# Kernel tuning notes

Measured on AMD Instinct MI355X. Metric: run time of the kernel, lower is better.

The kernel has to match this reference:

```python
import jax, jax.numpy as jnp
import numpy as np

FEATS = 1024
HEAD = 16
MLP_HIDDEN = 4096
HEAD_DIM = FEATS // HEAD
SQRT_D = float(FEATS) ** 0.5  # module scales by sqrt(feats), not sqrt(head_dim)
LN_EPS = 1e-5


def layer_norm(x, g, b):
    mu = jnp.mean(x, axis=-1, keepdims=True)
    var = jnp.mean(jnp.square(x - mu), axis=-1, keepdims=True)
    return (x - mu) * jax.lax.rsqrt(var + LN_EPS) * g + b


def setup_inputs() -> dict:
    key = jax.random.key(0)
    ks = jax.random.split(key, 12)
    s = 1.0 / np.sqrt(FEATS)
    s2 = 1.0 / np.sqrt(MLP_HIDDEN)
    return {
        "x": jax.random.normal(ks[0], (2, 2048, FEATS), dtype=jnp.float32),
        "ln1_g": jnp.ones((FEATS,), jnp.float32),
        "ln1_b": jnp.zeros((FEATS,), jnp.float32),
        "wq": jax.random.normal(ks[1], (FEATS, FEATS), jnp.float32) * s,
        "bq": jnp.zeros((FEATS,), jnp.float32),
        "wk": jax.random.normal(ks[2], (FEATS, FEATS), jnp.float32) * s,
        "bk": jnp.zeros((FEATS,), jnp.float32),
        "wv": jax.random.normal(ks[3], (FEATS, FEATS), jnp.float32) * s,
        "bv": jnp.zeros((FEATS,), jnp.float32),
        "wo": jax.random.normal(ks[4], (FEATS, FEATS), jnp.float32) * s,
        "bo": jnp.zeros((FEATS,), jnp.float32),
        "ln2_g": jnp.ones((FEATS,), jnp.float32),
        "ln2_b": jnp.zeros((FEATS,), jnp.float32),
        "w1": jax.random.normal(ks[5], (MLP_HIDDEN, FEATS), jnp.float32) * s,
        "b1": jnp.zeros((MLP_HIDDEN,), jnp.float32),
        "w2": jax.random.normal(ks[6], (FEATS, MLP_HIDDEN), jnp.float32) * s2,
        "b2": jnp.zeros((FEATS,), jnp.float32),
    }


def reference(x, ln1_g, ln1_b, wq, bq, wk, bk, wv, bv, wo, bo,
              ln2_g, ln2_b, w1, b1, w2, b2):
    b, n, f = x.shape
    h = layer_norm(x, ln1_g, ln1_b)
    # qkv projections (torch Linear: y = x @ W.T + b)
    q = (h @ wq.T + bq).reshape(b, n, HEAD, HEAD_DIM).transpose(0, 2, 1, 3)
    k = (h @ wk.T + bk).reshape(b, n, HEAD, HEAD_DIM).transpose(0, 2, 1, 3)
    v = (h @ wv.T + bv).reshape(b, n, HEAD, HEAD_DIM).transpose(0, 2, 1, 3)
    score = jax.nn.softmax(jnp.einsum('bhif,bhjf->bhij', q, k) / SQRT_D, axis=-1)
    attn = jnp.einsum('bhij,bhjf->bihf', score, v).reshape(b, n, f)
    o = attn @ wo.T + bo
    out1 = o + x
    h2 = layer_norm(out1, ln2_g, ln2_b)
    mlp = jax.nn.relu(jax.nn.relu(h2 @ w1.T + b1) @ w2.T + b2)
    return mlp + out1
```

## Files before the change

### kernel.cpp

```cpp
#include <hip/hip_runtime.h>
#include <hip/hip_bf16.h>

#define FEATS 1024
#define NH 16
#define HD 64
#define SEQ 2048
#define BATCH 2
#define MTOT (BATCH*SEQ)
#define MLPH 4096
#define QSCALE 0.04508422277369218f

typedef __attribute__((ext_vector_type(8))) short bf16x8;
typedef __attribute__((ext_vector_type(4))) short bf16x4;
typedef __attribute__((ext_vector_type(4))) float f32x4;

static_assert(sizeof(bf16x8) == 16, "bf16x8 must be 16B");

__device__ __forceinline__ unsigned short f2bf(float f) {
    unsigned int u = __float_as_uint(f);
    unsigned int lsb = (u >> 16) & 1u;
    u += 0x7fffu + lsb;
    return (unsigned short)(u >> 16);
}

#define ASYNC16(GP, LP) __builtin_amdgcn_global_load_lds( \
    (const __attribute__((address_space(1))) void*)(GP),  \
    (__attribute__((address_space(3))) void*)(LP), 16, 0, 0)

__global__ __launch_bounds__(256) void cvt_all_kernel(
    const float* __restrict__ wq, const float* __restrict__ wk,
    const float* __restrict__ wv, const float* __restrict__ wo,
    const float* __restrict__ w1, const float* __restrict__ w2,
    unsigned short* __restrict__ dst) {
    const size_t i = ((size_t)blockIdx.x * 256 + threadIdx.x) * 4;
    const size_t MB = (size_t)1024 * 1024;
    const float* s;
    size_t off;
    float sc = 1.0f;
    if (i < MB)            { s = wq; off = i;          sc = QSCALE; }
    else if (i < 2 * MB)   { s = wk; off = i - MB; }
    else if (i < 3 * MB)   { s = wv; off = i - 2 * MB; }
    else if (i < 4 * MB)   { s = wo; off = i - 3 * MB; }
    else if (i < 8 * MB)   { s = w1; off = i - 4 * MB; }
    else                   { s = w2; off = i - 8 * MB; }
    float4 v = *(const float4*)(s + off);
    ushort4 o;
    o.x = f2bf(v.x * sc); o.y = f2bf(v.y * sc);
    o.z = f2bf(v.z * sc); o.w = f2bf(v.w * sc);
    *(ushort4*)(dst + i) = o;
}

__global__ __launch_bounds__(256) void concat3_kernel(const float* __restrict__ a,
                                                      const float* __restrict__ b,
                                                      const float* __restrict__ c,
                                                      float* __restrict__ o) {
    int i = blockIdx.x * 256 + threadIdx.x;
    float v = (i < 1024) ? a[i] * QSCALE : ((i < 2048) ? b[i - 1024] : c[i - 2048]);
    o[i] = v;
}

__global__ __launch_bounds__(256) void ln_kernel(const float* __restrict__ x,
                                                 const float* __restrict__ g,
                                                 const float* __restrict__ bta,
                                                 unsigned short* __restrict__ h) {
    __shared__ float red[8];
    const int row = blockIdx.x;
    const int t = threadIdx.x;
    const float* xr = x + (size_t)row * FEATS;
    float4 v = ((const float4*)xr)[t];
    float s  = v.x + v.y + v.z + v.w;
    float ss = v.x * v.x + v.y * v.y + v.z * v.z + v.w * v.w;
#pragma unroll
    for (int off = 1; off < 64; off <<= 1) {
        s  += __shfl_xor(s, off);
        ss += __shfl_xor(ss, off);
    }
    const int w = t >> 6;
    if ((t & 63) == 0) { red[w] = s; red[4 + w] = ss; }
    __syncthreads();
    s  = red[0] + red[1] + red[2] + red[3];
    ss = red[4] + red[5] + red[6] + red[7];
    const float mu  = s * (1.f / FEATS);
    const float var = ss * (1.f / FEATS) - mu * mu;
    const float rs  = rsqrtf(var + 1e-5f);
    float4 gv = ((const float4*)g)[t];
    float4 bv = ((const float4*)bta)[t];
    ushort4 ov;
    ov.x = f2bf((v.x - mu) * rs * gv.x + bv.x);
    ov.y = f2bf((v.y - mu) * rs * gv.y + bv.y);
    ov.z = f2bf((v.z - mu) * rs * gv.z + bv.z);
    ov.w = f2bf((v.w - mu) * rs * gv.w + bv.w);
    ((ushort4*)h)[(size_t)row * (FEATS / 4) + t] = ov;
}

template <bool RELU, bool ADD, bool OUTBF16>
__global__ __launch_bounds__(256, 3)
void gemm_kernel(const unsigned short* __restrict__ A,
                 const unsigned short* __restrict__ W,
                 const float* __restrict__ bias,
                 const float* __restrict__ addend,
                 void* __restrict__ outp,
                 int M, int N, int K, int gx) {
    __shared__ unsigned short lds[3][2][128 * 32];

    const int t = threadIdx.x;
    const int w = t >> 6, lane = t & 63;
    const int wr = w >> 1, wc = w & 1;
    const int li = lane & 15, lj = lane >> 4;

    const int nwg = gridDim.x;
    const int cpx = nwg >> 3;
    const int wg = blockIdx.x;
    const int swz = (wg & 7) * cpx + (wg >> 3);
    const int mb = (swz / gx) * 128, nb = (swz % gx) * 128;

    const int srow = lane >> 2;
    const int scg = ((lane & 3) ^ (srow & 3)) * 8;
    const unsigned short* gA = A + (size_t)(mb + w * 16 + srow) * K + scg;
    const unsigned short* gB = W + (size_t)(nb + w * 16 + srow) * K + scg;
    const size_t half = (size_t)64 * K;
    const int lbase = w * 512 + lane * 8;

    const int rsw = (lj ^ (li & 3)) * 8;

    const int nt = K >> 5;

#define STAGE(BUF, K0)                                             \
    do {                                                           \
        unsigned short* la_ = &lds[BUF][0][lbase];                 \
        unsigned short* lb_ = &lds[BUF][1][lbase];                 \
        ASYNC16(gA + (K0), la_);                                   \
        ASYNC16(gA + half + (K0), la_ + 2048);                     \
        ASYNC16(gB + (K0), lb_);                                   \
        ASYNC16(gB + half + (K0), lb_ + 2048);                     \
    } while (0)

    STAGE(0, 0);
    STAGE(1, 32);
    asm volatile("s_waitcnt vmcnt(4)" ::: "memory");
    __builtin_amdgcn_s_barrier();

    f32x4 acc[4][4] = {};

    for (int i = 0; i < nt; ++i) {
        const int cur = i % 3;
        const unsigned short* Al = &lds[cur][0][0];
        const unsigned short* Bl = &lds[cur][1][0];

        bf16x8 af[4], bfr[4];
#pragma unroll
        for (int m = 0; m < 4; m++)
            af[m] = *(const bf16x8*)(Al + (wr * 64 + m * 16 + li) * 32 + rsw);
#pragma unroll
        for (int n = 0; n < 4; n++)
            bfr[n] = *(const bf16x8*)(Bl + (wc * 64 + n * 16 + li) * 32 + rsw);

        const int pf = i + 2 < nt;
        if (pf) STAGE((i + 2) % 3, (i + 2) * 32);

#pragma unroll
        for (int m = 0; m < 4; m++)
#pragma unroll
            for (int n = 0; n < 4; n++)
                acc[m][n] = __builtin_amdgcn_mfma_f32_16x16x32_bf16(af[m], bfr[n], acc[m][n], 0, 0, 0);

        if (i + 1 < nt) {
            if (pf) asm volatile("s_waitcnt vmcnt(4)" ::: "memory");
            else    asm volatile("s_waitcnt vmcnt(0)" ::: "memory");
            __builtin_amdgcn_s_barrier();
        }
    }
#undef STAGE

#pragma unroll
    for (int m = 0; m < 4; m++) {
#pragma unroll
        for (int n = 0; n < 4; n++) {
            const int col = nb + wc * 64 + n * 16 + li;
            const float bv = bias[col];
#pragma unroll
            for (int r = 0; r < 4; r++) {
                const int row = mb + wr * 64 + m * 16 + lj * 4 + r;
                float v = acc[m][n][r] + bv;
                if (RELU) v = fmaxf(v, 0.f);
                if (ADD)  v += addend[(size_t)row * N + col];
                if (OUTBF16)
                    ((unsigned short*)outp)[(size_t)row * N + col] = f2bf(v);
                else
                    ((float*)outp)[(size_t)row * N + col] = v;
            }
        }
    }
}

__global__ __launch_bounds__(256) void vtrans_kernel(const unsigned short* __restrict__ qkv,
                                                     unsigned short* __restrict__ vt) {
    constexpr int LDV = 68;
    __shared__ unsigned short Vl[64 * LDV];
    const int bh = blockIdx.x, st = blockIdx.y;
    const int b = bh >> 4, h = bh & 15;
    const int t = threadIdx.x;
    const unsigned short* src = qkv + (size_t)(b * SEQ + st * 64) * (3 * FEATS) + 2 * FEATS + h * HD;
#pragma unroll
    for (int i = 0; i < 2; i++) {
        int idx = t + i * 256;
        int r = idx >> 3, c = (idx & 7) * 8;
        *(bf16x8*)(Vl + r * LDV + c) = *(const bf16x8*)(src + (size_t)r * (3 * FEATS) + c);
    }
    __syncthreads();
    unsigned short* dst = vt + (size_t)bh * HD * SEQ + st * 64;
#pragma unroll
    for (int i = 0; i < 2; i++) {
        int idx = t + i * 256;
        int d = idx >> 3, s8 = (idx & 7) * 8;
        bf16x8 v;
#pragma unroll
        for (int j = 0; j < 8; j++) v[j] = Vl[(s8 + j) * LDV + d];
        *(bf16x8*)(dst + (size_t)d * SEQ + s8) = v;
    }
}

__global__ __launch_bounds__(512, 4)
void attn_kernel(const unsigned short* __restrict__ qkv,
                 const unsigned short* __restrict__ vt,
                 unsigned short* __restrict__ out) {
    constexpr int LK = 72;
    constexpr int LV = 136;
    __shared__ unsigned short Kl[2][128 * LK];
    __shared__ unsigned short Vtl[2][64 * LV];

    const int bh = blockIdx.x;
    const int b = bh >> 4, h = bh & 15;
    const int q0 = blockIdx.y * 128;
    const int t = threadIdx.x, w = t >> 6, lane = t & 63;
    const int li = lane & 15, lj = lane >> 4;

    const size_t rstr = 3 * FEATS;
    const unsigned short* qkvb = qkv + (size_t)(b * SEQ) * rstr;
    const unsigned short* ksrc = qkvb + FEATS + h * HD;
    const unsigned short* vsrc = vt + (size_t)bh * HD * SEQ;

    bf16x8 aq[2];
#pragma unroll
    for (int kk = 0; kk < 2; kk++)
        aq[kk] = *(const bf16x8*)(qkvb + (size_t)(q0 + w * 16 + li) * rstr + h * HD + kk * 32 + lj * 8);

    f32x4 o[4] = {};
    float lsum = 0.f;

    const int skey = t >> 2, sc = (t & 3) * 16;
    const unsigned short* kg = ksrc + (size_t)skey * rstr + sc;
    const int ldoK = skey * LK + sc;
    const int sd = t >> 3, c0 = (t & 7) * 16;
    const unsigned short* vg = vsrc + (size_t)sd * SEQ + c0;
    const int posA = (c0 & 96) | (((c0 >> 2) & 3) << 3) | (((c0 >> 4) & 1) << 2);
    const int ldoV = sd * LV + posA;

    const int nt = SEQ / 128;

#define VSPLIT(VR0, VR1, BUF)                                            \
    do {                                                                 \
        *(bf16x4*)(&Vtl[BUF][ldoV])      = __builtin_shufflevector(VR0, VR0, 0, 1, 2, 3); \
        *(bf16x4*)(&Vtl[BUF][ldoV + 8])  = __builtin_shufflevector(VR0, VR0, 4, 5, 6, 7); \
        *(bf16x4*)(&Vtl[BUF][ldoV + 16]) = __builtin_shufflevector(VR1, VR1, 0, 1, 2, 3); \
        *(bf16x4*)(&Vtl[BUF][ldoV + 24]) = __builtin_shufflevector(VR1, VR1, 4, 5, 6, 7); \
    } while (0)

    {
        bf16x8 k0 = *(const bf16x8*)kg;
        bf16x8 k1 = *(const bf16x8*)(kg + 8);
        bf16x8 v0 = *(const bf16x8*)vg;
        bf16x8 v1 = *(const bf16x8*)(vg + 8);
        *(bf16x8*)(&Kl[0][ldoK])     = k0;
        *(bf16x8*)(&Kl[0][ldoK + 8]) = k1;
        VSPLIT(v0, v1, 0);
    }

    int cur = 0;
    for (int i = 0; i < nt; ++i) {
        bf16x8 kr0, kr1, vr0, vr1;
        if (i + 1 < nt) {
            const unsigned short* kn = kg + (size_t)(i + 1) * 128 * rstr;
            const unsigned short* vn = vg + (i + 1) * 128;
            kr0 = *(const bf16x8*)kn;
            kr1 = *(const bf16x8*)(kn + 8);
            vr0 = *(const bf16x8*)vn;
            vr1 = *(const bf16x8*)(vn + 8);
        }

        asm volatile("s_waitcnt lgkmcnt(0)" ::: "memory");
        __builtin_amdgcn_s_barrier();

        const unsigned short* Kc = Kl[cur];
        const unsigned short* Vc = Vtl[cur];

        f32x4 s[8];
        __builtin_amdgcn_s_setprio(1);
#pragma unroll
        for (int n = 0; n < 8; n++) {
            bf16x8 k0 = *(const bf16x8*)(Kc + (n * 16 + li) * LK + lj * 8);
            bf16x8 k1 = *(const bf16x8*)(Kc + (n * 16 + li) * LK + 32 + lj * 8);
            f32x4 acc = {};
            acc = __builtin_amdgcn_mfma_f32_16x16x32_bf16(k0, aq[0], acc, 0, 0, 0);
            acc = __builtin_amdgcn_mfma_f32_16x16x32_bf16(k1, aq[1], acc, 0, 0, 0);
            s[n] = acc;
        }
        __builtin_amdgcn_s_setprio(0);

        bf16x8 A[4];
#pragma unroll
        for (int kk = 0; kk < 4; kk++) {
            float p[8];
#pragma unroll
            for (int r = 0; r < 4; r++) {
                p[r]     = exp2f(s[2 * kk][r]);
                p[4 + r] = exp2f(s[2 * kk + 1][r]);
                lsum += p[r] + p[4 + r];
            }
            union { unsigned u[4]; bf16x8 v; } Au;
            asm("v_cvt_pk_bf16_f32 %0, %1, %2" : "=v"(Au.u[0]) : "v"(p[0]), "v"(p[1]));
            asm("v_cvt_pk_bf16_f32 %0, %1, %2" : "=v"(Au.u[1]) : "v"(p[2]), "v"(p[3]));
            asm("v_cvt_pk_bf16_f32 %0, %1, %2" : "=v"(Au.u[2]) : "v"(p[4]), "v"(p[5]));
            asm("v_cvt_pk_bf16_f32 %0, %1, %2" : "=v"(Au.u[3]) : "v"(p[6]), "v"(p[7]));
            A[kk] = Au.v;
        }

        __builtin_amdgcn_s_setprio(1);
#pragma unroll
        for (int n = 0; n < 4; n++) {
#pragma unroll
            for (int kk = 0; kk < 4; kk++) {
                bf16x8 bv = *(const bf16x8*)(Vc + (n * 16 + li) * LV + kk * 32 + lj * 8);
                o[n] = __builtin_amdgcn_mfma_f32_16x16x32_bf16(A[kk], bv, o[n], 0, 0, 0);
            }
        }
        __builtin_amdgcn_s_setprio(0);

        if (i + 1 < nt) {
            *(bf16x8*)(&Kl[cur ^ 1][ldoK])     = kr0;
            *(bf16x8*)(&Kl[cur ^ 1][ldoK + 8]) = kr1;
            VSPLIT(vr0, vr1, cur ^ 1);
        }
        cur ^= 1;
    }
#undef VSPLIT

    lsum += __shfl_xor(lsum, 16);
    lsum += __shfl_xor(lsum, 32);
    const float dinv = 1.f / lsum;
    float inv[4];
#pragma unroll
    for (int r = 0; r < 4; r++)
        inv[r] = __shfl(dinv, lj * 4 + r);

    unsigned short* ob = out + (size_t)(b * SEQ + q0 + w * 16) * FEATS + h * HD;
#pragma unroll
    for (int n = 0; n < 4; n++)
#pragma unroll
        for (int r = 0; r < 4; r++)
            ob[(size_t)(lj * 4 + r) * FEATS + n * 16 + li] = f2bf(o[n][r] * inv[r]);
}

extern "C" void kernel_launch(void* const* d_in, const int* in_sizes, int n_in,
                              void* d_out, int out_size, void* d_ws, size_t ws_size,
                              hipStream_t stream) {
    const float* x     = (const float*)d_in[0];
    const float* ln1_g = (const float*)d_in[1];
    const float* ln1_b = (const float*)d_in[2];
    const float* wq    = (const float*)d_in[3];
    const float* bq    = (const float*)d_in[4];
    const float* wk    = (const float*)d_in[5];
    const float* bk    = (const float*)d_in[6];
    const float* wv    = (const float*)d_in[7];
    const float* bvv   = (const float*)d_in[8];
    const float* wo    = (const float*)d_in[9];
    const float* bo    = (const float*)d_in[10];
    const float* ln2_g = (const float*)d_in[11];
    const float* ln2_b = (const float*)d_in[12];
    const float* w1    = (const float*)d_in[13];
    const float* b1    = (const float*)d_in[14];
    const float* w2    = (const float*)d_in[15];
    const float* b2    = (const float*)d_in[16];

    unsigned short* wqkv_b = (unsigned short*)d_ws;
    unsigned short* wo_b   = wqkv_b + 3072 * 1024;
    unsigned short* w1_b   = wo_b + 1024 * 1024;
    unsigned short* w2_b   = w1_b + 4096 * 1024;
    float*          bqkv   = (float*)(w2_b + 1024 * 4096);
    unsigned short* region = (unsigned short*)(bqkv + 3072);
    unsigned short* qkvb   = region;
    unsigned short* hb     = region + (size_t)4096 * 3072;
    unsigned short* vtb    = hb;
    unsigned short* a1     = region;
    unsigned short* attn_o = region + (size_t)4096 * 4096;
    unsigned short* h2     = attn_o;
    float*          out1   = (float*)(attn_o + (size_t)4096 * 1024);
    float*          outf   = (float*)d_out;

    dim3 blk(256);

    cvt_all_kernel<<<12288, blk, 0, stream>>>(wq, wk, wv, wo, w1, w2, wqkv_b);
    concat3_kernel<<<12, blk, 0, stream>>>(bq, bk, bvv, bqkv);

    ln_kernel<<<MTOT, blk, 0, stream>>>(x, ln1_g, ln1_b, hb);

    gemm_kernel<false, false, true><<<768, blk, 0, stream>>>(
        hb, wqkv_b, bqkv, nullptr, qkvb, MTOT, 3072, FEATS, 24);

    vtrans_kernel<<<dim3(BATCH * NH, SEQ / 64), blk, 0, stream>>>(qkvb, vtb);

    attn_kernel<<<dim3(BATCH * NH, SEQ / 128), dim3(512), 0, stream>>>(qkvb, vtb, attn_o);

    gemm_kernel<false, true, false><<<256, blk, 0, stream>>>(
        attn_o, wo_b, bo, x, out1, MTOT, FEATS, FEATS, 8);

    ln_kernel<<<MTOT, blk, 0, stream>>>(out1, ln2_g, ln2_b, h2);

    gemm_kernel<true, false, true><<<1024, blk, 0, stream>>>(
        h2, w1_b, b1, nullptr, a1, MTOT, MLPH, FEATS, 32);

    gemm_kernel<true, true, false><<<256, blk, 0, stream>>>(
        a1, w2_b, b2, out1, outf, MTOT, FEATS, MLPH, 8);
}
```

Measured before the change: 236.0 us.

## Halve attention block to 4 waves each handling 32 query rows

The attention kernel now launches 256 threads instead of 512, and each wave processes two 16-row query tiles. Each K and V fragment read from LDS is therefore reused across two MFMA streams, and each thread loads twice as much K/V per tile. The row-sum of probabilities is now computed with an extra MFMA against a vector of ones instead of scalar adds and cross-lane shuffles, and it is summed over the bf16-rounded probabilities. The cost is higher register pressure per wave and fewer waves per block available to hide latency.

```diff
diff --git a/kernel.cpp b/kernel.cpp
--- a/kernel.cpp
+++ b/kernel.cpp
@@ -220,7 +220,7 @@
     }
 }
 
-__global__ __launch_bounds__(512, 4)
+__global__ __launch_bounds__(256, 2)
 void attn_kernel(const unsigned short* __restrict__ qkv,
                  const unsigned short* __restrict__ vt,
                  unsigned short* __restrict__ out) {
@@ -240,52 +240,76 @@
     const unsigned short* ksrc = qkvb + FEATS + h * HD;
     const unsigned short* vsrc = vt + (size_t)bh * HD * SEQ;
 
-    bf16x8 aq[2];
-#pragma unroll
-    for (int kk = 0; kk < 2; kk++)
-        aq[kk] = *(const bf16x8*)(qkvb + (size_t)(q0 + w * 16 + li) * rstr + h * HD + kk * 32 + lj * 8);
-
-    f32x4 o[4] = {};
-    float lsum = 0.f;
-
-    const int skey = t >> 2, sc = (t & 3) * 16;
-    const unsigned short* kg = ksrc + (size_t)skey * rstr + sc;
-    const int ldoK = skey * LK + sc;
-    const int sd = t >> 3, c0 = (t & 7) * 16;
-    const unsigned short* vg = vsrc + (size_t)sd * SEQ + c0;
-    const int posA = (c0 & 96) | (((c0 >> 2) & 3) << 3) | (((c0 >> 4) & 1) << 2);
-    const int ldoV = sd * LV + posA;
+    bf16x8 aq[2][2];
+#pragma unroll
+    for (int hh = 0; hh < 2; hh++)
+#pragma unroll
+        for (int kk = 0; kk < 2; kk++)
+            aq[hh][kk] = *(const bf16x8*)(qkvb +
+                (size_t)(q0 + w * 32 + hh * 16 + li) * rstr + h * HD + kk * 32 + lj * 8);
+
+    f32x4 o[2][4] = {};
+    f32x4 oS[2] = {};
+
+    const short onebf = (short)0x3F80;
+    const bf16x8 ones = {onebf, onebf, onebf, onebf, onebf, onebf, onebf, onebf};
+
+    const int skey = t >> 1, dbase = (t & 1) * 32;
+    const unsigned short* kg = ksrc + (size_t)skey * rstr + dbase;
+    const int ldoK = skey * LK + dbase;
+    const int sd = t >> 2, kbase = (t & 3) * 32;
+    const unsigned short* vg = vsrc + (size_t)sd * SEQ + kbase;
+    const int ldoV = sd * LV + kbase;
 
     const int nt = SEQ / 128;
 
-#define VSPLIT(VR0, VR1, BUF)                                            \
-    do {                                                                 \
-        *(bf16x4*)(&Vtl[BUF][ldoV])      = __builtin_shufflevector(VR0, VR0, 0, 1, 2, 3); \
-        *(bf16x4*)(&Vtl[BUF][ldoV + 8])  = __builtin_shufflevector(VR0, VR0, 4, 5, 6, 7); \
-        *(bf16x4*)(&Vtl[BUF][ldoV + 16]) = __builtin_shufflevector(VR1, VR1, 0, 1, 2, 3); \
-        *(bf16x4*)(&Vtl[BUF][ldoV + 24]) = __builtin_shufflevector(VR1, VR1, 4, 5, 6, 7); \
+#define KW(BUF, R0, R1, R2, R3)                          \
+    do {                                                 \
+        *(bf16x8*)(&Kl[BUF][ldoK])      = R0;            \
+        *(bf16x8*)(&Kl[BUF][ldoK + 8])  = R1;            \
+        *(bf16x8*)(&Kl[BUF][ldoK + 16]) = R2;            \
+        *(bf16x8*)(&Kl[BUF][ldoK + 24]) = R3;            \
+    } while (0)
+#define VW1(BUF, VR, POS)                                                              \
+    do {                                                                               \
+        *(bf16x4*)(&Vtl[BUF][(POS)])     = __builtin_shufflevector(VR, VR, 0, 1, 2, 3);\
+        *(bf16x4*)(&Vtl[BUF][(POS) + 8]) = __builtin_shufflevector(VR, VR, 4, 5, 6, 7);\
+    } while (0)
+#define VW(BUF, V0, V1, V2, V3)                          \
+    do {                                                 \
+        VW1(BUF, V0, ldoV);                              \
+        VW1(BUF, V1, ldoV + 16);                         \
+        VW1(BUF, V2, ldoV + 4);                          \
+        VW1(BUF, V3, ldoV + 20);                         \
     } while (0)
 
     {
         bf16x8 k0 = *(const bf16x8*)kg;
         bf16x8 k1 = *(const bf16x8*)(kg + 8);
+        bf16x8 k2 = *(const bf16x8*)(kg + 16);
+        bf16x8 k3 = *(const bf16x8*)(kg + 24);
         bf16x8 v0 = *(const bf16x8*)vg;
         bf16x8 v1 = *(const bf16x8*)(vg + 8);
-        *(bf16x8*)(&Kl[0][ldoK])     = k0;
-        *(bf16x8*)(&Kl[0][ldoK + 8]) = k1;
-        VSPLIT(v0, v1, 0);
+        bf16x8 v2 = *(const bf16x8*)(vg + 16);
+        bf16x8 v3 = *(const bf16x8*)(vg + 24);
+        KW(0, k0, k1, k2, k3);
+        VW(0, v0, v1, v2, v3);
     }
 
     int cur = 0;
     for (int i = 0; i < nt; ++i) {
-        bf16x8 kr0, kr1, vr0, vr1;
+        bf16x8 kr0, kr1, kr2, kr3, vr0, vr1, vr2, vr3;
         if (i + 1 < nt) {
             const unsigned short* kn = kg + (size_t)(i + 1) * 128 * rstr;
             const unsigned short* vn = vg + (i + 1) * 128;
             kr0 = *(const bf16x8*)kn;
             kr1 = *(const bf16x8*)(kn + 8);
+            kr2 = *(const bf16x8*)(kn + 16);
+            kr3 = *(const bf16x8*)(kn + 24);
             vr0 = *(const bf16x8*)vn;
             vr1 = *(const bf16x8*)(vn + 8);
+            vr2 = *(const bf16x8*)(vn + 16);
+            vr3 = *(const bf16x8*)(vn + 24);
         }
 
         asm volatile("s_waitcnt lgkmcnt(0)" ::: "memory");
@@ -294,36 +318,46 @@
         const unsigned short* Kc = Kl[cur];
         const unsigned short* Vc = Vtl[cur];
 
-        f32x4 s[8];
+        f32x4 s[2][8];
         __builtin_amdgcn_s_setprio(1);
 #pragma unroll
         for (int n = 0; n < 8; n++) {
             bf16x8 k0 = *(const bf16x8*)(Kc + (n * 16 + li) * LK + lj * 8);
             bf16x8 k1 = *(const bf16x8*)(Kc + (n * 16 + li) * LK + 32 + lj * 8);
-            f32x4 acc = {};
-            acc = __builtin_amdgcn_mfma_f32_16x16x32_bf16(k0, aq[0], acc, 0, 0, 0);
-            acc = __builtin_amdgcn_mfma_f32_16x16x32_bf16(k1, aq[1], acc, 0, 0, 0);
-            s[n] = acc;
+#pragma unroll
+            for (int hh = 0; hh < 2; hh++) {
+                f32x4 acc = {};
+                acc = __builtin_amdgcn_mfma_f32_16x16x32_bf16(k0, aq[hh][0], acc, 0, 0, 0);
+                acc = __builtin_amdgcn_mfma_f32_16x16x32_bf16(k1, aq[hh][1], acc, 0, 0, 0);
+                s[hh][n] = acc;
+            }
         }
         __builtin_amdgcn_s_setprio(0);
 
-        bf16x8 A[4];
-#pragma unroll
-        for (int kk = 0; kk < 4; kk++) {
-            float p[8];
-#pragma unroll
-            for (int r = 0; r < 4; r++) {
-                p[r]     = exp2f(s[2 * kk][r]);
-                p[4 + r] = exp2f(s[2 * kk + 1][r]);
-                lsum += p[r] + p[4 + r];
+        bf16x8 A[2][4];
+#pragma unroll
+        for (int hh = 0; hh < 2; hh++)
+#pragma unroll
+            for (int kk = 0; kk < 4; kk++) {
+                float p[8];
+#pragma unroll
+                for (int r = 0; r < 4; r++) {
+                    p[r]     = exp2f(s[hh][2 * kk][r]);
+                    p[4 + r] = exp2f(s[hh][2 * kk + 1][r]);
+                }
+                union { unsigned u[4]; bf16x8 v; } Au;
+                asm("v_cvt_pk_bf16_f32 %0, %1, %2" : "=v"(Au.u[0]) : "v"(p[0]), "v"(p[1]));
+                asm("v_cvt_pk_bf16_f32 %0, %1, %2" : "=v"(Au.u[1]) : "v"(p[2]), "v"(p[3]));
+                asm("v_cvt_pk_bf16_f32 %0, %1, %2" : "=v"(Au.u[2]) : "v"(p[4]), "v"(p[5]));
+                asm("v_cvt_pk_bf16_f32 %0, %1, %2" : "=v"(Au.u[3]) : "v"(p[6]), "v"(p[7]));
+                A[hh][kk] = Au.v;
             }
-            union { unsigned u[4]; bf16x8 v; } Au;
-            asm("v_cvt_pk_bf16_f32 %0, %1, %2" : "=v"(Au.u[0]) : "v"(p[0]), "v"(p[1]));
-            asm("v_cvt_pk_bf16_f32 %0, %1, %2" : "=v"(Au.u[1]) : "v"(p[2]), "v"(p[3]));
-            asm("v_cvt_pk_bf16_f32 %0, %1, %2" : "=v"(Au.u[2]) : "v"(p[4]), "v"(p[5]));
-            asm("v_cvt_pk_bf16_f32 %0, %1, %2" : "=v"(Au.u[3]) : "v"(p[6]), "v"(p[7]));
-            A[kk] = Au.v;
-        }
+
+#pragma unroll
+        for (int hh = 0; hh < 2; hh++)
+#pragma unroll
+            for (int kk = 0; kk < 4; kk++)
+                oS[hh] = __builtin_amdgcn_mfma_f32_16x16x32_bf16(A[hh][kk], ones, oS[hh], 0, 0, 0);
 
         __builtin_amdgcn_s_setprio(1);
 #pragma unroll
@@ -331,34 +365,33 @@
 #pragma unroll
             for (int kk = 0; kk < 4; kk++) {
                 bf16x8 bv = *(const bf16x8*)(Vc + (n * 16 + li) * LV + kk * 32 + lj * 8);
-                o[n] = __builtin_amdgcn_mfma_f32_16x16x32_bf16(A[kk], bv, o[n], 0, 0, 0);
+                o[0][n] = __builtin_amdgcn_mfma_f32_16x16x32_bf16(A[0][kk], bv, o[0][n], 0, 0, 0);
+                o[1][n] = __builtin_amdgcn_mfma_f32_16x16x32_bf16(A[1][kk], bv, o[1][n], 0, 0, 0);
             }
         }
         __builtin_amdgcn_s_setprio(0);
 
         if (i + 1 < nt) {
-            *(bf16x8*)(&Kl[cur ^ 1][ldoK])     = kr0;
-            *(bf16x8*)(&Kl[cur ^ 1][ldoK + 8]) = kr1;
-            VSPLIT(vr0, vr1, cur ^ 1);
+            KW(cur ^ 1, kr0, kr1, kr2, kr3);
+            VW(cur ^ 1, vr0, vr1, vr2, vr3);
         }
         cur ^= 1;
     }
-#undef VSPLIT
-
-    lsum += __shfl_xor(lsum, 16);
-    lsum += __shfl_xor(lsum, 32);
-    const float dinv = 1.f / lsum;
-    float inv[4];
-#pragma unroll
-    for (int r = 0; r < 4; r++)
-        inv[r] = __shfl(dinv, lj * 4 + r);
-
-    unsigned short* ob = out + (size_t)(b * SEQ + q0 + w * 16) * FEATS + h * HD;
-#pragma unroll
-    for (int n = 0; n < 4; n++)
-#pragma unroll
-        for (int r = 0; r < 4; r++)
-            ob[(size_t)(lj * 4 + r) * FEATS + n * 16 + li] = f2bf(o[n][r] * inv[r]);
+#undef KW
+#undef VW
+#undef VW1
+
+    unsigned short* ob = out + (size_t)(b * SEQ + q0 + w * 32) * FEATS + h * HD;
+#pragma unroll
+    for (int hh = 0; hh < 2; hh++)
+#pragma unroll
+        for (int r = 0; r < 4; r++) {
+            const float inv = 1.f / oS[hh][r];
+#pragma unroll
+            for (int n = 0; n < 4; n++)
+                ob[(size_t)(hh * 16 + lj * 4 + r) * FEATS + n * 16 + li] =
+                    f2bf(o[hh][n][r] * inv);
+        }
 }
 
 extern "C" void kernel_launch(void* const* d_in, const int* in_sizes, int n_in,
@@ -409,7 +442,7 @@
 
     vtrans_kernel<<<dim3(BATCH * NH, SEQ / 64), blk, 0, stream>>>(qkvb, vtb);
 
-    attn_kernel<<<dim3(BATCH * NH, SEQ / 128), dim3(512), 0, stream>>>(qkvb, vtb, attn_o);
+    attn_kernel<<<dim3(BATCH * NH, SEQ / 128), dim3(256), 0, stream>>>(qkvb, vtb, attn_o);
 
     gemm_kernel<false, true, false><<<256, blk, 0, stream>>>(
         attn_o, wo_b, bo, x, out1, MTOT, FEATS, FEATS, 8);
```

Measured after the change: 232.7 us. No clear change (-1.4%).
